# Performance work log

Hardware: AMD Instinct MI355X
Metric: run time of the kernel (lower is better)

The kernel has to match this reference:

```python
import jax, jax.numpy as jnp
import numpy as np

WS = 2          # spatial window (patch) size
C = 96          # patch channels
IMG = 256       # image size
NS = IMG // WS  # 128 patches per side
N = NS * NS     # 16384 tokens
TD = C * WS * WS  # 384 token dim
H = 6           # heads
D = TD // H     # 64 head dim
W1 = 128        # one-sided attention window (attention_window=256 // 2)
G = 50          # num global tokens
NEG = -1e9
GPOS = np.linspace(0, N - 1, G).astype(np.int32)  # torch.linspace(...).long()


def setup_inputs() -> dict:
    key = jax.random.key(0)
    ks = jax.random.split(key, 13)
    s = 1.0 / np.sqrt(TD)
    def W(k):
        return jax.random.normal(k, (TD, TD), jnp.float32) * s
    def b(k):
        return jax.random.normal(k, (TD,), jnp.float32) * 0.02
    return {
        'x': jax.random.normal(ks[0], (2, C, IMG, IMG), jnp.float32),
        'Wq': W(ks[1]), 'bq': b(ks[2]),
        'Wk': W(ks[3]), 'bk': b(ks[4]),
        'Wv': W(ks[5]), 'bv': b(ks[6]),
        'Wqg': W(ks[7]), 'bqg': b(ks[8]),
        'Wkg': W(ks[9]), 'bkg': b(ks[10]),
        'Wvg': W(ks[11]), 'bvg': b(ks[12]),
    }


def _tokens(x):
    # (B,C,IMG,IMG) -> (B,N,TD); matches unfold/permute/view of the torch code
    B = x.shape[0]
    t = x.reshape(B, C, NS, WS, NS, WS).transpose(0, 1, 2, 4, 3, 5)  # B,C,ns,ns,ws,ws
    t = t.reshape(B, C, N, WS * WS).transpose(0, 2, 1, 3)
    return t.reshape(B, N, TD)


def _untokens(o):
    B = o.shape[0]
    o = o.reshape(B, NS, NS, C, WS, WS).transpose(0, 3, 1, 4, 2, 5)
    return o.reshape(B, C, IMG, IMG)


def _heads(t):
    B = t.shape[0]
    return t.reshape(B, -1, H, D).transpose(0, 2, 1, 3)  # (B,H,S,D)


def _longformer(tokens, Wq, bq, Wk, bk, Wv, bv, Wqg, bqg, Wkg, bkg, Wvg, bvg):
    B = tokens.shape[0]
    scale = np.float32(1.0 / np.sqrt(D))
    q = _heads(tokens @ Wq + bq) * scale  # (B,H,N,D)
    k = _heads(tokens @ Wk + bk)
    v = _heads(tokens @ Wv + bv)

    nc = N // W1  # 128 chunks of size w
    qc = q.reshape(B, H, nc, W1, D)
    # overlapping key/value chunks of size 3w (prev | cur | next)
    kp = jnp.pad(k, ((0, 0), (0, 0), (W1, W1), (0, 0))).reshape(B, H, nc + 2, W1, D)
    vp = jnp.pad(v, ((0, 0), (0, 0), (W1, W1), (0, 0))).reshape(B, H, nc + 2, W1, D)
    k3 = jnp.concatenate([kp[:, :, :-2], kp[:, :, 1:-1], kp[:, :, 2:]], axis=3)  # (B,H,nc,3w,D)
    v3 = jnp.concatenate([vp[:, :, :-2], vp[:, :, 1:-1], vp[:, :, 2:]], axis=3)

    band = jnp.einsum('bhcqd,bhckd->bhcqk', qc, k3)  # (B,H,nc,w,3w)
    # banded validity: key within +-w of query, and inside [0,N)
    i = np.arange(W1)[:, None]
    j = np.arange(3 * W1)[None, :]
    rel = j - W1 - i
    relmask = (rel >= -W1) & (rel <= W1)  # (w,3w)
    absidx = np.arange(nc)[:, None] * W1 + np.arange(3 * W1)[None, :] - W1
    absmask = (absidx >= 0) & (absidx < N)  # (nc,3w)
    mask = jnp.asarray(relmask[None, :, :] & absmask[:, None, :])  # (nc,w,3w)
    band = jnp.where(mask[None, None], band, NEG)

    # global key columns seen by every (local) query
    kg = k[:, :, GPOS]  # (B,H,G,D)
    vg = v[:, :, GPOS]
    gsc = jnp.einsum('bhcqd,bhgd->bhcqg', qc, kg)  # (B,H,nc,w,G)

    probs = jax.nn.softmax(jnp.concatenate([gsc, band], axis=-1), axis=-1)
    out = jnp.einsum('bhcqg,bhgd->bhcqd', probs[..., :G], vg) \
        + jnp.einsum('bhcqk,bhckd->bhcqd', probs[..., G:], v3)
    out = out.reshape(B, H, N, D).transpose(0, 2, 1, 3).reshape(B, N, TD)

    # global-query full attention (separate projections), overwrite global rows
    qg = _heads((tokens[:, GPOS] @ Wqg + bqg)) * scale  # (B,H,G,D)
    kga = _heads(tokens @ Wkg + bkg)  # (B,H,N,D)
    vga = _heads(tokens @ Wvg + bvg)
    gp = jax.nn.softmax(jnp.einsum('bhgd,bhnd->bhgn', qg, kga), axis=-1)
    og = jnp.einsum('bhgn,bhnd->bhgd', gp, vga).transpose(0, 2, 1, 3).reshape(B, G, TD)
    return out.at[:, GPOS].set(og)


def reference(x, Wq, bq, Wk, bk, Wv, bv, Wqg, bqg, Wkg, bkg, Wvg, bvg):
    tokens = _tokens(x)
    out = _longformer(tokens, Wq, bq, Wk, bk, Wv, bv, Wqg, bqg, Wkg, bkg, Wvg, bvg)
    return _untokens(out)
```

## Files before the change

### kernel.cpp

```cpp
#include <hip/hip_runtime.h>

#define DEVI __device__ __forceinline__

typedef __bf16 v8bf __attribute__((ext_vector_type(8)));
typedef float f32x4 __attribute__((ext_vector_type(4)));
typedef int int4v __attribute__((ext_vector_type(4)));
typedef int int2v __attribute__((ext_vector_type(2)));

constexpr int B_  = 2;
constexpr int C_  = 96;
constexpr int IMG = 256;
constexpr int N_  = 16384;
constexpr int TD  = 384;
constexpr int H_  = 6;
constexpr int G_  = 50;

DEVI short f2bf(float f){
  unsigned u = __builtin_bit_cast(unsigned, f);
  u = (u + 0x7fffu + ((u >> 16) & 1u)) >> 16;
  return (short)u;
}
DEVI unsigned cvtpk(float lo, float hi){
  unsigned r;
  asm("v_cvt_pk_bf16_f32 %0, %1, %2" : "=v"(r) : "v"(lo), "v"(hi));
  return r;
}
DEVI int gpos(int g){ return (16383 * g) / 49; }

DEVI f32x4 mfma16(v8bf a, v8bf b, f32x4 c){
  return __builtin_amdgcn_mfma_f32_16x16x32_bf16(a, b, c, 0, 0, 0);
}

DEVI void gload16(const void* g, void* l){
  __builtin_amdgcn_global_load_lds((const __attribute__((address_space(1))) void*)g,
                                   (__attribute__((address_space(3))) void*)l, 16, 0, 0);
}

__global__ void prep_w(const float* __restrict__ w0, const float* __restrict__ w1,
                       const float* __restrict__ w2, const float* __restrict__ w3,
                       const float* __restrict__ w4, const float* __restrict__ w5,
                       short* __restrict__ Wt){
  int z = blockIdx.y;
  const float* W = z==0 ? w0 : z==1 ? w1 : z==2 ? w2 : z==3 ? w3 : z==4 ? w4 : w5;
  int idx = blockIdx.x * 256 + threadIdx.x;
  int n = idx / TD, k = idx % TD;
  Wt[z*TD*TD + idx] = f2bf(W[k*TD + n]);
}

__global__ void tokenize(const float* __restrict__ x, short* __restrict__ tokens){
  int idx = blockIdx.x * 256 + threadIdx.x;
  int t8 = idx % (TD/8);
  int bn = idx / (TD/8);
  int n = bn % N_, b = bn / N_;
  int t0 = t8 * 8;
  int i0 = (n >> 7) * 2, j0 = (n & 127) * 2;
  short o[8];
  #pragma unroll
  for (int e = 0; e < 8; e++){
    int t = t0 + e;
    int c = t >> 2, wi = (t >> 1) & 1, wj = t & 1;
    o[e] = f2bf(x[((b*C_ + c)*IMG + i0 + wi)*IMG + j0 + wj]);
  }
  *reinterpret_cast<int4v*>(tokens + bn*TD + t0) = *reinterpret_cast<int4v*>(o);
}

__global__ void gather_tokg(const short* __restrict__ tokens, short* __restrict__ tokg){
  int idx = blockIdx.x*256 + threadIdx.x;
  int r = idx / 48, cb = (idx % 48)*8;
  int b = r >> 6, q = r & 63;
  int4v val = {};
  if (q < G_) val = *reinterpret_cast<const int4v*>(tokens + ((size_t)b*N_ + gpos(q))*TD + cb);
  *reinterpret_cast<int4v*>(tokg + r*TD + cb) = val;
}

__global__ __launch_bounds__(256) void gemm_proj(
    const short* __restrict__ A, const short* __restrict__ Wt,
    const float* __restrict__ bq, const float* __restrict__ bk, const float* __restrict__ bv,
    const float* __restrict__ bkg, const float* __restrict__ bvg,
    short* __restrict__ qbuf, short* __restrict__ kbuf, short* __restrict__ vT,
    short* __restrict__ kgabuf, short* __restrict__ vgaT)
{
  __shared__ short smem[16384];
  int lin = blockIdx.x;
  int id = (lin & 7)*480 + (lin >> 3);
  int mt = id / 15, r15 = id % 15;
  int by = r15 % 3, bz = r15 / 3;
  const float* bias = bz==0 ? bq : bz==1 ? bk : bz==2 ? bv : bz==3 ? bkg : bvg;
  const short* Wz = Wt + bz*TD*TD;
  int m0 = mt * 128, n0 = by * 128;
  int tid = threadIdx.x, l = tid & 63, w = tid >> 6;
  int wm = w >> 1, wn = w & 1;

  int st_r  = (l >> 2);
  int st_cg = ((l & 3) ^ ((l >> 3) & 3));
  auto STAGE = [&](int kt, int s){
    #pragma unroll
    for (int it = 0; it < 4; it++){
      int ch = w*4 + it;
      int c8 = ch & 7;
      int r_ = c8*16 + st_r;
      const short* src = (ch < 8)
        ? A  + (size_t)(m0+r_)*TD + kt*32 + st_cg*8
        : Wz + (size_t)(n0+r_)*TD + kt*32 + st_cg*8;
      gload16(src, smem + ((ch < 8) ? 0 : 8192) + s*4096 + c8*512);
    }
  };

  int fr = l & 15;
  int fcg = (l >> 4) ^ ((l >> 1) & 3);
  f32x4 acc[4][4] = {};

  STAGE(0, 0);
  __syncthreads();
  #pragma unroll 2
  for (int t = 0; t < 12; t++){
    int cur = t & 1;
    if (t + 1 < 12) STAGE(t+1, cur ^ 1);
    v8bf af[4], bfr[4];
    #pragma unroll
    for (int i = 0; i < 4; i++){
      af[i]  = *reinterpret_cast<const v8bf*>(&smem[       cur*4096 + (wm*64 + i*16 + fr)*32 + fcg*8]);
      bfr[i] = *reinterpret_cast<const v8bf*>(&smem[8192 + cur*4096 + (wn*64 + i*16 + fr)*32 + fcg*8]);
    }
    #pragma unroll
    for (int mi = 0; mi < 4; mi++)
      #pragma unroll
      for (int ni = 0; ni < 4; ni++)
        acc[mi][ni] = mfma16(af[mi], bfr[ni], acc[mi][ni]);
    __syncthreads();
  }

  if (bz == 2 || bz == 4){
    short* outT = (bz == 2) ? vT : vgaT;
    #pragma unroll
    for (int mi = 0; mi < 4; mi++){
      int n_base = wm*64 + mi*16 + (l>>4)*4;
      #pragma unroll
      for (int ni = 0; ni < 4; ni++){
        int t_local = wn*64 + ni*16 + (l&15);
        float bc = bias[n0 + t_local];
        short pk[4];
        #pragma unroll
        for (int jj = 0; jj < 4; jj++) pk[jj] = f2bf(acc[mi][ni][jj] + bc);
        int phys = t_local*128 + (((n_base >> 3) ^ (t_local & 15)) << 3) + (n_base & 7);
        *reinterpret_cast<int2v*>(&smem[phys]) = *reinterpret_cast<int2v*>(pk);
      }
    }
    __syncthreads();
    int b = mt >> 7;
    int nb = m0 & 16383;
    #pragma unroll
    for (int p = 0; p < 8; p++){
      int t = p*16 + (tid >> 4);
      int c8 = tid & 15;
      int4v val = *reinterpret_cast<const int4v*>(&smem[t*128 + ((c8 ^ (t & 15)) << 3)]);
      int h = (n0 + t) >> 6, d = (n0 + t) & 63;
      *reinterpret_cast<int4v*>(outT + ((size_t)((b*H_ + h)*64 + d))*N_ + nb + c8*8) = val;
    }
  } else {
    short* out = bz==0 ? qbuf : bz==1 ? kbuf : kgabuf;
    float scale = (bz == 0) ? 0.125f : 1.0f;
    #pragma unroll
    for (int mi = 0; mi < 4; mi++){
      int row = m0 + wm*64 + mi*16 + (l>>4)*4;
      #pragma unroll
      for (int ni = 0; ni < 4; ni++){
        int col = n0 + wn*64 + ni*16 + (l&15);
        float bc = bias[col];
        #pragma unroll
        for (int jj = 0; jj < 4; jj++)
          out[(size_t)(row+jj)*TD + col] = f2bf((acc[mi][ni][jj] + bc) * scale);
      }
    }
  }
}

__global__ __launch_bounds__(256) void gemm_qg(
    const short* __restrict__ A, const short* __restrict__ Wt,
    const float* __restrict__ bias, short* __restrict__ out)
{
  __shared__ short sA[128][72];
  __shared__ short sB[128][72];
  const short* Wz = Wt + 5*TD*TD;
  int n0 = blockIdx.x * 128;
  int tid = threadIdx.x, l = tid & 63, w = tid >> 6;
  int wm = w >> 1, wn = w & 1;
  f32x4 acc[4][4] = {};
  for (int k0 = 0; k0 < TD; k0 += 64){
    #pragma unroll
    for (int i = 0; i < 4; i++){
      int ch = i*256 + tid; int row = ch >> 3, cb = (ch & 7) * 8;
      *reinterpret_cast<int4v*>(&sA[row][cb]) = *reinterpret_cast<const int4v*>(A  + row*TD + k0 + cb);
      *reinterpret_cast<int4v*>(&sB[row][cb]) = *reinterpret_cast<const int4v*>(Wz + (n0+row)*TD + k0 + cb);
    }
    __syncthreads();
    #pragma unroll
    for (int ks = 0; ks < 2; ks++){
      v8bf af[4], bfr[4];
      #pragma unroll
      for (int i = 0; i < 4; i++){
        af[i]  = *reinterpret_cast<const v8bf*>(&sA[wm*64 + i*16 + (l&15)][ks*32 + (l>>4)*8]);
        bfr[i] = *reinterpret_cast<const v8bf*>(&sB[wn*64 + i*16 + (l&15)][ks*32 + (l>>4)*8]);
      }
      #pragma unroll
      for (int mi = 0; mi < 4; mi++)
        #pragma unroll
        for (int ni = 0; ni < 4; ni++)
          acc[mi][ni] = mfma16(af[mi], bfr[ni], acc[mi][ni]);
    }
    __syncthreads();
  }
  #pragma unroll
  for (int mi = 0; mi < 4; mi++){
    int row = wm*64 + mi*16 + (l>>4)*4;
    #pragma unroll
    for (int ni = 0; ni < 4; ni++){
      int col = n0 + wn*64 + ni*16 + (l&15);
      float bc = bias[col];
      #pragma unroll
      for (int jj = 0; jj < 4; jj++)
        out[(row+jj)*TD + col] = f2bf((acc[mi][ni][jj] + bc) * 0.125f);
    }
  }
}

__global__ void gather_gkv(const short* __restrict__ kbuf, const short* __restrict__ vT,
                           short* __restrict__ kg, short* __restrict__ vgTg){
  int bh = blockIdx.x; int b = bh / H_, h = bh % H_;
  int t = threadIdx.x;
  #pragma unroll
  for (int it = 0; it < 2; it++){
    int u = it*256 + t; int g = u >> 3, cc = (u & 7)*8;
    int4v val = {};
    if (g < G_) val = *reinterpret_cast<const int4v*>(kbuf + ((size_t)b*N_ + gpos(g))*TD + h*64 + cc);
    *reinterpret_cast<int4v*>(kg + (size_t)bh*4096 + g*64 + cc) = val;
  }
  #pragma unroll
  for (int it = 0; it < 16; it++){
    int u = it*256 + t; int d = u >> 6, g = u & 63;
    short val = 0;
    if (g < G_) val = vT[((size_t)bh*64 + d)*N_ + gpos(g)];
    vgTg[(size_t)bh*4096 + d*64 + g] = val;
  }
}

__global__ __launch_bounds__(512, 4) void band_attn(
    const short* __restrict__ qb, const short* __restrict__ kbuf, const short* __restrict__ vT,
    const short* __restrict__ kg, const short* __restrict__ vgTg,
    float* __restrict__ out)
{
  __shared__ short sK[448][64];
  __shared__ short sP[8][16][72];
  int lin = blockIdx.y*128 + blockIdx.x;
  int id = (lin & 7)*192 + (lin >> 3);
  int c = id & 127;
  int bh = id >> 7; int b = bh / H_, h = bh % H_;
  int tid = threadIdx.x, l = tid & 63, w = tid >> 6;
  int g4 = l >> 4, q16 = l & 15;
  int cb0 = c*128 - 128;

  #pragma unroll
  for (int it = 0; it < 7; it++){
    int ch = w*7 + it;
    int r = ch*8 + (l>>3), cc = (l&7)*8;
    const short* src;
    if (ch < 8){
      src = kg + (size_t)bh*4096 + r*64 + cc;
    } else {
      int ka = cb0 + r - 64;
      ka = ka < 0 ? 0 : (ka > N_-1 ? N_-1 : ka);
      src = kbuf + ((size_t)b*N_ + ka)*TD + h*64 + cc;
    }
    gload16(src, &sK[ch*8][0]);
  }

  int qrow0 = c*128 + w*16;
  v8bf aq[2];
  #pragma unroll
  for (int s = 0; s < 2; s++)
    aq[s] = *reinterpret_cast<const v8bf*>(qb + ((size_t)b*N_ + qrow0 + q16)*TD + h*64 + s*32 + g4*8);

  __syncthreads();

  f32x4 o[4] = {};
  float mrun = -1e30f, lrun = 0.f;

  int sbase = w >> 2;
  for (int sidx = 0; sidx < 6; sidx++){
    bool isg = (sidx == 0);
    int s0b = (sbase + sidx - 1) * 64;
    int kabs0 = cb0 + s0b;
    if (!isg && (kabs0 < 0 || kabs0 >= N_)) continue;
    int rbase = isg ? 0 : 64 + s0b;
    v8bf bv0[4];
    #pragma unroll
    for (int cf = 0; cf < 4; cf++){
      const short* vsrc = isg
        ? vgTg + (size_t)bh*4096 + (cf*16 + q16)*64 + g4*8
        : vT + ((size_t)bh*64 + cf*16 + q16)*N_ + kabs0 + g4*8;
      bv0[cf] = *reinterpret_cast<const v8bf*>(vsrc);
    }
    v8bf bkf[4][2];
    #pragma unroll
    for (int kc = 0; kc < 4; kc++)
      #pragma unroll
      for (int s = 0; s < 2; s++)
        bkf[kc][s] = *reinterpret_cast<const v8bf*>(&sK[rbase + kc*16 + q16][s*32 + g4*8]);
    f32x4 sc[4] = {};
    __builtin_amdgcn_s_setprio(1);
    #pragma unroll
    for (int kc = 0; kc < 4; kc++){
      sc[kc] = mfma16(bkf[kc][0], aq[0], sc[kc]);
      sc[kc] = mfma16(bkf[kc][1], aq[1], sc[kc]);
    }
    __builtin_amdgcn_s_setprio(0);
    if (isg){
      #pragma unroll
      for (int jj = 0; jj < 4; jj++)
        if (48 + g4*4 + jj >= G_) sc[3][jj] = -1e30f;
    } else {
      bool allv = (s0b >= w*16 + 15) && (s0b <= w*16 + 193);
      if (!allv){
        int i_ = w*16 + q16;
        #pragma unroll
        for (int kc = 0; kc < 4; kc++)
          #pragma unroll
          for (int jj = 0; jj < 4; jj++){
            int rel = s0b + kc*16 + g4*4 + jj - 128 - i_;
            if (rel < -128 || rel > 128) sc[kc][jj] = -1e30f;
          }
      }
    }
    float mk = -1e30f;
    #pragma unroll
    for (int kc = 0; kc < 4; kc++)
      #pragma unroll
      for (int jj = 0; jj < 4; jj++) mk = fmaxf(mk, sc[kc][jj]);
    mk = fmaxf(mk, __shfl_xor(mk, 16, 64));
    mk = fmaxf(mk, __shfl_xor(mk, 32, 64));
    float mnew = fmaxf(mrun, mk);
    float f_ = __expf(mrun - mnew);
    mrun = mnew;
    float s_ = 0.f;
    #pragma unroll
    for (int kc = 0; kc < 4; kc++){
      #pragma unroll
      for (int jj = 0; jj < 4; jj++){
        sc[kc][jj] = __expf(sc[kc][jj] - mnew);
        s_ += sc[kc][jj];
      }
      int2v pw = { (int)cvtpk(sc[kc][0], sc[kc][1]), (int)cvtpk(sc[kc][2], sc[kc][3]) };
      *reinterpret_cast<int2v*>(&sP[w][q16][kc*16 + g4*4]) = pw;
    }
    s_ += __shfl_xor(s_, 16, 64);
    s_ += __shfl_xor(s_, 32, 64);
    lrun = lrun*f_ + s_;
    #pragma unroll
    for (int cf = 0; cf < 4; cf++)
      #pragma unroll
      for (int jj = 0; jj < 4; jj++) o[cf][jj] *= f_;
    v8bf ap[2];
    #pragma unroll
    for (int s2 = 0; s2 < 2; s2++)
      ap[s2] = *reinterpret_cast<const v8bf*>(&sP[w][q16][s2*32 + g4*8]);
    v8bf bv1[4];
    #pragma unroll
    for (int cf = 0; cf < 4; cf++){
      const short* vsrc = isg
        ? vgTg + (size_t)bh*4096 + (cf*16 + q16)*64 + 32 + g4*8
        : vT + ((size_t)bh*64 + cf*16 + q16)*N_ + kabs0 + 32 + g4*8;
      bv1[cf] = *reinterpret_cast<const v8bf*>(vsrc);
    }
    __builtin_amdgcn_s_setprio(1);
    #pragma unroll
    for (int cf = 0; cf < 4; cf++) o[cf] = mfma16(bv0[cf], ap[0], o[cf]);
    #pragma unroll
    for (int cf = 0; cf < 4; cf++) o[cf] = mfma16(bv1[cf], ap[1], o[cf]);
    __builtin_amdgcn_s_setprio(0);
  }
  float inv = 1.0f / lrun;
  int n = qrow0 + q16;
  int i0 = (n >> 7)*2, j0 = (n & 127)*2;
  #pragma unroll
  for (int cf = 0; cf < 4; cf++)
    #pragma unroll
    for (int jj = 0; jj < 4; jj++){
      float val = o[cf][jj] * inv;
      int t_ = h*64 + cf*16 + g4*4 + jj;
      int cc = t_ >> 2, wi = (t_ >> 1) & 1, wj = t_ & 1;
      out[((b*C_ + cc)*IMG + i0 + wi)*IMG + j0 + wj] = val;
    }
}

__global__ __launch_bounds__(256) void gattn_partial(
    const short* __restrict__ qgb, const short* __restrict__ kga, const short* __restrict__ vgaT,
    float* __restrict__ gpart)
{
  __shared__ short sP[4][64][72];
  int bh = blockIdx.x; int b = bh / H_, h = bh % H_;
  int kc = blockIdx.y;
  int tid = threadIdx.x, l = tid & 63, w = tid >> 6;
  v8bf aq[4][2];
  #pragma unroll
  for (int rf = 0; rf < 4; rf++)
    #pragma unroll
    for (int s = 0; s < 2; s++)
      aq[rf][s] = *reinterpret_cast<const v8bf*>(qgb + (b*64 + rf*16 + (l&15))*TD + h*64 + s*32 + (l>>4)*8);
  f32x4 o[4][4] = {};
  float mrun[4][4], lrun[4][4];
  #pragma unroll
  for (int rf = 0; rf < 4; rf++)
    #pragma unroll
    for (int jj = 0; jj < 4; jj++){ mrun[rf][jj] = -1e30f; lrun[rf][jj] = 0.f; }
  int keybase = kc*1024 + w*256;
  for (int st = 0; st < 4; st++){
    int key0 = keybase + st*64;
    v8bf bkf[4][2];
    #pragma unroll
    for (int kc2 = 0; kc2 < 4; kc2++)
      #pragma unroll
      for (int s = 0; s < 2; s++)
        bkf[kc2][s] = *reinterpret_cast<const v8bf*>(kga + ((size_t)b*N_ + key0 + kc2*16 + (l&15))*TD + h*64 + s*32 + (l>>4)*8);
    #pragma unroll
    for (int rf = 0; rf < 4; rf++){
      f32x4 sc[4] = {};
      #pragma unroll
      for (int kc2 = 0; kc2 < 4; kc2++){
        sc[kc2] = mfma16(aq[rf][0], bkf[kc2][0], sc[kc2]);
        sc[kc2] = mfma16(aq[rf][1], bkf[kc2][1], sc[kc2]);
      }
      #pragma unroll
      for (int jj = 0; jj < 4; jj++){
        float mk = fmaxf(fmaxf(sc[0][jj], sc[1][jj]), fmaxf(sc[2][jj], sc[3][jj]));
        #pragma unroll
        for (int off = 1; off < 16; off <<= 1) mk = fmaxf(mk, __shfl_xor(mk, off, 64));
        float mnew = fmaxf(mrun[rf][jj], mk);
        float f_ = __expf(mrun[rf][jj] - mnew);
        mrun[rf][jj] = mnew;
        float p0 = __expf(sc[0][jj]-mnew), p1 = __expf(sc[1][jj]-mnew);
        float p2 = __expf(sc[2][jj]-mnew), p3 = __expf(sc[3][jj]-mnew);
        float s_ = (p0+p1)+(p2+p3);
        #pragma unroll
        for (int off = 1; off < 16; off <<= 1) s_ += __shfl_xor(s_, off, 64);
        lrun[rf][jj] = lrun[rf][jj]*f_ + s_;
        #pragma unroll
        for (int cf = 0; cf < 4; cf++) o[rf][cf][jj] *= f_;
        int pr = rf*16 + (l>>4)*4 + jj;
        sP[w][pr][(l&15)]    = f2bf(p0);
        sP[w][pr][16+(l&15)] = f2bf(p1);
        sP[w][pr][32+(l&15)] = f2bf(p2);
        sP[w][pr][48+(l&15)] = f2bf(p3);
      }
    }
    #pragma unroll
    for (int cf = 0; cf < 4; cf++){
      #pragma unroll
      for (int s2 = 0; s2 < 2; s2++){
        v8bf bv = *reinterpret_cast<const v8bf*>(vgaT + ((size_t)bh*64 + cf*16 + (l&15))*N_ + key0 + s2*32 + (l>>4)*8);
        #pragma unroll
        for (int rf = 0; rf < 4; rf++){
          v8bf ap = *reinterpret_cast<const v8bf*>(&sP[w][rf*16 + (l&15)][s2*32 + (l>>4)*8]);
          o[rf][cf] = mfma16(ap, bv, o[rf][cf]);
        }
      }
    }
  }
  float* base = gpart + (size_t)(bh*64 + kc*4 + w) * 4224;
  #pragma unroll
  for (int rf = 0; rf < 4; rf++){
    #pragma unroll
    for (int jj = 0; jj < 4; jj++){
      int q = rf*16 + (l>>4)*4 + jj;
      if ((l & 15) == 0){ base[q] = mrun[rf][jj]; base[64 + q] = lrun[rf][jj]; }
    }
    #pragma unroll
    for (int cf = 0; cf < 4; cf++)
      *reinterpret_cast<f32x4*>(&base[128 + (cf*16 + (l&15))*64 + rf*16 + (l>>4)*4]) = o[rf][cf];
  }
}

__global__ void gattn_combine(const float* __restrict__ gpart, float* __restrict__ out){
  int bh = blockIdx.x; int b = bh / H_, h = bh % H_;
  int quarter = blockIdx.y;
  int t = threadIdx.x;
  int q = t & 63, dq = t >> 6;
  if (q >= G_) return;
  const float* pb = gpart + (size_t)bh * 64 * 4224;
  float M = -1e30f;
  for (int p = 0; p < 64; p++) M = fmaxf(M, pb[p*4224 + q]);
  float L = 0.f; float acc[4] = {};
  int d0 = quarter*16 + dq*4;
  for (int p = 0; p < 64; p++){
    const float* pp = pb + p*4224;
    float wgt = __expf(pp[q] - M);
    L += pp[64 + q] * wgt;
    #pragma unroll
    for (int e = 0; e < 4; e++) acc[e] += pp[128 + (d0+e)*64 + q] * wgt;
  }
  float invL = 1.0f / L;
  int n = gpos(q);
  int i0 = (n >> 7)*2, j0 = (n & 127)*2;
  #pragma unroll
  for (int e = 0; e < 4; e++){
    int t_ = h*64 + d0 + e;
    int cc = t_ >> 2, wi = (t_ >> 1) & 1, wj = t_ & 1;
    out[((b*C_ + cc)*IMG + i0 + wi)*IMG + j0 + wj] = acc[e] * invL;
  }
}

extern "C" void kernel_launch(void* const* d_in, const int* in_sizes, int n_in,
                              void* d_out, int out_size, void* d_ws, size_t ws_size,
                              hipStream_t stream)
{
  (void)in_sizes; (void)n_in; (void)out_size; (void)ws_size;
  const float* x   = (const float*)d_in[0];
  const float* Wq  = (const float*)d_in[1];  const float* bq  = (const float*)d_in[2];
  const float* Wk  = (const float*)d_in[3];  const float* bk  = (const float*)d_in[4];
  const float* Wv  = (const float*)d_in[5];  const float* bv  = (const float*)d_in[6];
  const float* Wqg = (const float*)d_in[7];  const float* bqg = (const float*)d_in[8];
  const float* Wkg = (const float*)d_in[9];  const float* bkg = (const float*)d_in[10];
  const float* Wvg = (const float*)d_in[11]; const float* bvg = (const float*)d_in[12];
  float* out = (float*)d_out;

  short* ws = (short*)d_ws;
  const size_t SZ = (size_t)B_ * N_ * TD;
  short* tokens  = ws;
  short* Wt      = tokens  + SZ;
  short* tokg    = Wt      + (size_t)6*TD*TD;
  short* qgb     = tokg    + (size_t)128*TD;
  short* qbuf    = qgb     + (size_t)128*TD;
  short* kbuf    = qbuf    + SZ;
  short* kgabuf  = kbuf    + SZ;
  short* vT      = kgabuf  + SZ;
  short* vgaT    = vT      + SZ;
  short* kg      = vgaT    + SZ;
  short* vgTg    = kg      + (size_t)12*64*64;
  float* gpart   = (float*)tokens;

  prep_w<<<dim3(576,6), dim3(256), 0, stream>>>(Wq, Wk, Wv, Wkg, Wvg, Wqg, Wt);
  tokenize<<<dim3(6144), dim3(256), 0, stream>>>(x, tokens);
  gemm_proj<<<dim3(3840), dim3(256), 0, stream>>>(tokens, Wt, bq, bk, bv, bkg, bvg,
                                                  qbuf, kbuf, vT, kgabuf, vgaT);
  gather_tokg<<<dim3(24), dim3(256), 0, stream>>>(tokens, tokg);
  gemm_qg<<<dim3(3), dim3(256), 0, stream>>>(tokg, Wt, bqg, qgb);
  gather_gkv<<<dim3(12), dim3(256), 0, stream>>>(kbuf, vT, kg, vgTg);
  band_attn<<<dim3(128,12), dim3(512), 0, stream>>>(qbuf, kbuf, vT, kg, vgTg, out);
  gattn_partial<<<dim3(12,16), dim3(256), 0, stream>>>(qgb, kgabuf, vgaT, gpart);
  gattn_combine<<<dim3(12,4), dim3(256), 0, stream>>>(gpart, out);
}
```

Measured before the change: 249.1 us.

## Tile weight transpose, relax GEMM barriers, transpose global-attention MFMA layout

Three changes land together. The weight prep kernel now transposes through a 64x64 LDS tile, so both its reads and writes are coalesced. The projection GEMM's K loop swaps __syncthreads for explicit vmcnt/lgkmcnt waits plus raw barriers, so the next stage's async LDS loads overlap the current MFMAs. The global-attention partial kernel swaps MFMA operand order so each lane owns one query row, which cuts the softmax reductions to two shuffles and writes P with packed bf16 conversions. The hand-written waitcnt values are fragile if the number of loads per stage ever changes.

Measured after the change: 232.3 us. -6.8%, faster.

```diff
diff --git a/kernel.cpp b/kernel.cpp
--- a/kernel.cpp
+++ b/kernel.cpp
@@ -36,15 +36,32 @@
                                    (__attribute__((address_space(3))) void*)l, 16, 0, 0);
 }
 
-__global__ void prep_w(const float* __restrict__ w0, const float* __restrict__ w1,
-                       const float* __restrict__ w2, const float* __restrict__ w3,
-                       const float* __restrict__ w4, const float* __restrict__ w5,
-                       short* __restrict__ Wt){
+__global__ __launch_bounds__(256) void prep_w(
+    const float* __restrict__ w0, const float* __restrict__ w1,
+    const float* __restrict__ w2, const float* __restrict__ w3,
+    const float* __restrict__ w4, const float* __restrict__ w5,
+    short* __restrict__ Wt){
+  __shared__ float sT[64][65];
   int z = blockIdx.y;
   const float* W = z==0 ? w0 : z==1 ? w1 : z==2 ? w2 : z==3 ? w3 : z==4 ? w4 : w5;
-  int idx = blockIdx.x * 256 + threadIdx.x;
-  int n = idx / TD, k = idx % TD;
-  Wt[z*TD*TD + idx] = f2bf(W[k*TD + n]);
+  int tile = blockIdx.x;
+  int k0 = (tile / 6) * 64, n0 = (tile % 6) * 64;
+  int t = threadIdx.x;
+  int r = t >> 2, c0 = (t & 3) * 16;
+  #pragma unroll
+  for (int e = 0; e < 16; e += 4){
+    f32x4 v = *reinterpret_cast<const f32x4*>(&W[(size_t)(k0+r)*TD + n0 + c0 + e]);
+    #pragma unroll
+    for (int i = 0; i < 4; i++) sT[r][c0 + e + i] = v[i];
+  }
+  __syncthreads();
+  int rn = t >> 2, ck0 = (t & 3) * 16;
+  short pk[16];
+  #pragma unroll
+  for (int e = 0; e < 16; e++) pk[e] = f2bf(sT[ck0 + e][rn]);
+  short* dst = Wt + (size_t)z*TD*TD + (size_t)(n0+rn)*TD + k0 + ck0;
+  *reinterpret_cast<int4v*>(dst)     = *reinterpret_cast<int4v*>(&pk[0]);
+  *reinterpret_cast<int4v*>(dst + 8) = *reinterpret_cast<int4v*>(&pk[8]);
 }
 
 __global__ void tokenize(const float* __restrict__ x, short* __restrict__ tokens){
@@ -111,11 +128,16 @@
   f32x4 acc[4][4] = {};
 
   STAGE(0, 0);
-  __syncthreads();
   #pragma unroll 2
   for (int t = 0; t < 12; t++){
     int cur = t & 1;
-    if (t + 1 < 12) STAGE(t+1, cur ^ 1);
+    if (t < 11){
+      STAGE(t+1, cur ^ 1);
+      asm volatile("s_waitcnt vmcnt(4)" ::: "memory");
+    } else {
+      asm volatile("s_waitcnt vmcnt(0)" ::: "memory");
+    }
+    __builtin_amdgcn_s_barrier();
     v8bf af[4], bfr[4];
     #pragma unroll
     for (int i = 0; i < 4; i++){
@@ -127,7 +149,8 @@
       #pragma unroll
       for (int ni = 0; ni < 4; ni++)
         acc[mi][ni] = mfma16(af[mi], bfr[ni], acc[mi][ni]);
-    __syncthreads();
+    asm volatile("s_waitcnt lgkmcnt(0)" ::: "memory");
+    __builtin_amdgcn_s_barrier();
   }
 
   if (bz == 2 || bz == 4){
@@ -400,82 +423,91 @@
   int bh = blockIdx.x; int b = bh / H_, h = bh % H_;
   int kc = blockIdx.y;
   int tid = threadIdx.x, l = tid & 63, w = tid >> 6;
+  int g4 = l >> 4, q16 = l & 15;
   v8bf aq[4][2];
   #pragma unroll
   for (int rf = 0; rf < 4; rf++)
     #pragma unroll
     for (int s = 0; s < 2; s++)
-      aq[rf][s] = *reinterpret_cast<const v8bf*>(qgb + (b*64 + rf*16 + (l&15))*TD + h*64 + s*32 + (l>>4)*8);
+      aq[rf][s] = *reinterpret_cast<const v8bf*>(qgb + (b*64 + rf*16 + q16)*TD + h*64 + s*32 + g4*8);
   f32x4 o[4][4] = {};
-  float mrun[4][4], lrun[4][4];
-  #pragma unroll
-  for (int rf = 0; rf < 4; rf++)
-    #pragma unroll
-    for (int jj = 0; jj < 4; jj++){ mrun[rf][jj] = -1e30f; lrun[rf][jj] = 0.f; }
+  float mrun[4], lrun[4];
+  #pragma unroll
+  for (int rf = 0; rf < 4; rf++){ mrun[rf] = -1e30f; lrun[rf] = 0.f; }
   int keybase = kc*1024 + w*256;
   for (int st = 0; st < 4; st++){
     int key0 = keybase + st*64;
     v8bf bkf[4][2];
     #pragma unroll
-    for (int kc2 = 0; kc2 < 4; kc2++)
+    for (int kcf = 0; kcf < 4; kcf++)
       #pragma unroll
       for (int s = 0; s < 2; s++)
-        bkf[kc2][s] = *reinterpret_cast<const v8bf*>(kga + ((size_t)b*N_ + key0 + kc2*16 + (l&15))*TD + h*64 + s*32 + (l>>4)*8);
+        bkf[kcf][s] = *reinterpret_cast<const v8bf*>(kga + ((size_t)b*N_ + key0 + kcf*16 + q16)*TD + h*64 + s*32 + g4*8);
     #pragma unroll
     for (int rf = 0; rf < 4; rf++){
       f32x4 sc[4] = {};
       #pragma unroll
-      for (int kc2 = 0; kc2 < 4; kc2++){
-        sc[kc2] = mfma16(aq[rf][0], bkf[kc2][0], sc[kc2]);
-        sc[kc2] = mfma16(aq[rf][1], bkf[kc2][1], sc[kc2]);
-      }
-      #pragma unroll
-      for (int jj = 0; jj < 4; jj++){
-        float mk = fmaxf(fmaxf(sc[0][jj], sc[1][jj]), fmaxf(sc[2][jj], sc[3][jj]));
-        #pragma unroll
-        for (int off = 1; off < 16; off <<= 1) mk = fmaxf(mk, __shfl_xor(mk, off, 64));
-        float mnew = fmaxf(mrun[rf][jj], mk);
-        float f_ = __expf(mrun[rf][jj] - mnew);
-        mrun[rf][jj] = mnew;
-        float p0 = __expf(sc[0][jj]-mnew), p1 = __expf(sc[1][jj]-mnew);
-        float p2 = __expf(sc[2][jj]-mnew), p3 = __expf(sc[3][jj]-mnew);
-        float s_ = (p0+p1)+(p2+p3);
-        #pragma unroll
-        for (int off = 1; off < 16; off <<= 1) s_ += __shfl_xor(s_, off, 64);
-        lrun[rf][jj] = lrun[rf][jj]*f_ + s_;
-        #pragma unroll
-        for (int cf = 0; cf < 4; cf++) o[rf][cf][jj] *= f_;
-        int pr = rf*16 + (l>>4)*4 + jj;
-        sP[w][pr][(l&15)]    = f2bf(p0);
-        sP[w][pr][16+(l&15)] = f2bf(p1);
-        sP[w][pr][32+(l&15)] = f2bf(p2);
-        sP[w][pr][48+(l&15)] = f2bf(p3);
-      }
-    }
-    #pragma unroll
-    for (int cf = 0; cf < 4; cf++){
-      #pragma unroll
-      for (int s2 = 0; s2 < 2; s2++){
-        v8bf bv = *reinterpret_cast<const v8bf*>(vgaT + ((size_t)bh*64 + cf*16 + (l&15))*N_ + key0 + s2*32 + (l>>4)*8);
-        #pragma unroll
-        for (int rf = 0; rf < 4; rf++){
-          v8bf ap = *reinterpret_cast<const v8bf*>(&sP[w][rf*16 + (l&15)][s2*32 + (l>>4)*8]);
-          o[rf][cf] = mfma16(ap, bv, o[rf][cf]);
+      for (int kcf = 0; kcf < 4; kcf++){
+        sc[kcf] = mfma16(bkf[kcf][0], aq[rf][0], sc[kcf]);
+        sc[kcf] = mfma16(bkf[kcf][1], aq[rf][1], sc[kcf]);
+      }
+      float mk = -1e30f;
+      #pragma unroll
+      for (int kcf = 0; kcf < 4; kcf++)
+        #pragma unroll
+        for (int jj = 0; jj < 4; jj++) mk = fmaxf(mk, sc[kcf][jj]);
+      mk = fmaxf(mk, __shfl_xor(mk, 16, 64));
+      mk = fmaxf(mk, __shfl_xor(mk, 32, 64));
+      float mnew = fmaxf(mrun[rf], mk);
+      float f_ = __expf(mrun[rf] - mnew);
+      mrun[rf] = mnew;
+      float s_ = 0.f;
+      #pragma unroll
+      for (int kcf = 0; kcf < 4; kcf++){
+        #pragma unroll
+        for (int jj = 0; jj < 4; jj++){
+          sc[kcf][jj] = __expf(sc[kcf][jj] - mnew);
+          s_ += sc[kcf][jj];
         }
+        int2v pw = { (int)cvtpk(sc[kcf][0], sc[kcf][1]), (int)cvtpk(sc[kcf][2], sc[kcf][3]) };
+        *reinterpret_cast<int2v*>(&sP[w][rf*16 + q16][kcf*16 + g4*4]) = pw;
+      }
+      s_ += __shfl_xor(s_, 16, 64);
+      s_ += __shfl_xor(s_, 32, 64);
+      lrun[rf] = lrun[rf]*f_ + s_;
+      #pragma unroll
+      for (int cf = 0; cf < 4; cf++)
+        #pragma unroll
+        for (int jj = 0; jj < 4; jj++) o[rf][cf][jj] *= f_;
+    }
+    v8bf bv[4][2];
+    #pragma unroll
+    for (int cf = 0; cf < 4; cf++)
+      #pragma unroll
+      for (int s2 = 0; s2 < 2; s2++)
+        bv[cf][s2] = *reinterpret_cast<const v8bf*>(vgaT + ((size_t)bh*64 + cf*16 + q16)*N_ + key0 + s2*32 + g4*8);
+    #pragma unroll
+    for (int rf = 0; rf < 4; rf++){
+      v8bf ap[2];
+      #pragma unroll
+      for (int s2 = 0; s2 < 2; s2++)
+        ap[s2] = *reinterpret_cast<const v8bf*>(&sP[w][rf*16 + q16][s2*32 + g4*8]);
+      #pragma unroll
+      for (int cf = 0; cf < 4; cf++){
+        o[rf][cf] = mfma16(bv[cf][0], ap[0], o[rf][cf]);
+        o[rf][cf] = mfma16(bv[cf][1], ap[1], o[rf][cf]);
       }
     }
   }
   float* base = gpart + (size_t)(bh*64 + kc*4 + w) * 4224;
   #pragma unroll
   for (int rf = 0; rf < 4; rf++){
-    #pragma unroll
-    for (int jj = 0; jj < 4; jj++){
-      int q = rf*16 + (l>>4)*4 + jj;
-      if ((l & 15) == 0){ base[q] = mrun[rf][jj]; base[64 + q] = lrun[rf][jj]; }
-    }
+    if (g4 == 0){ base[rf*16 + q16] = mrun[rf]; base[64 + rf*16 + q16] = lrun[rf]; }
     #pragma unroll
     for (int cf = 0; cf < 4; cf++)
-      *reinterpret_cast<f32x4*>(&base[128 + (cf*16 + (l&15))*64 + rf*16 + (l>>4)*4]) = o[rf][cf];
+      #pragma unroll
+      for (int jj = 0; jj < 4; jj++)
+        base[128 + (cf*16 + g4*4 + jj)*64 + rf*16 + q16] = o[rf][cf][jj];
   }
 }
 
@@ -537,7 +569,7 @@
   short* vgTg    = kg      + (size_t)12*64*64;
   float* gpart   = (float*)tokens;
 
-  prep_w<<<dim3(576,6), dim3(256), 0, stream>>>(Wq, Wk, Wv, Wkg, Wvg, Wqg, Wt);
+  prep_w<<<dim3(36,6), dim3(256), 0, stream>>>(Wq, Wk, Wv, Wkg, Wvg, Wqg, Wt);
   tokenize<<<dim3(6144), dim3(256), 0, stream>>>(x, tokens);
   gemm_proj<<<dim3(3840), dim3(256), 0, stream>>>(tokens, Wt, bq, bk, bv, bkg, bvg,
                                                   qbuf, kbuf, vT, kgabuf, vgaT);
```
